# Kernel optimization log

Hardware: AMD Instinct MI355X
Metric: run time of the kernel (lower is better)

Reference implementation:

```python
import jax, jax.numpy as jnp
import numpy as np

N_PATCHES = 14  # per side -> 196 patches

def patchify(images, n_patches):
    # images: [n, c, h, w]; returns [n, n_patches**2, c*ps*ps] with flatten order (c, ph, pw)
    n, c, h, w = images.shape
    ps = h // n_patches
    x = images.reshape(n, c, n_patches, ps, n_patches, ps)
    x = x.transpose(0, 2, 4, 1, 3, 5)  # [n, np_i, np_j, c, ps, ps]
    return x.reshape(n, n_patches * n_patches, c * ps * ps)

def setup_inputs() -> dict:
    key = jax.random.key(0)
    k1, k2, k3, k4 = jax.random.split(key, 4)
    B, C, H, Wd = 64, 3, 224, 224
    input_d = C * (H // N_PATCHES) * (Wd // N_PATCHES)  # 768
    hidden_d = 768
    images = jax.random.normal(k1, (B, C, H, Wd), dtype=jnp.float32)
    W = jax.random.normal(k2, (hidden_d, input_d), dtype=jnp.float32) * (1.0 / np.sqrt(input_d))
    b = jax.random.normal(k3, (hidden_d,), dtype=jnp.float32) * 0.01
    class_token = jax.random.uniform(k4, (1, hidden_d), dtype=jnp.float32)
    return {"images": images, "W": W, "b": b, "class_token": class_token}

def reference(images, W, b, class_token):
    patches = patchify(images, N_PATCHES)               # [B, 196, 768]
    tokens = jnp.einsum('bpd,hd->bph', patches, W) + b  # linear_mapper
    B = tokens.shape[0]
    cls = jnp.broadcast_to(class_token[None, :, :], (B, 1, class_token.shape[-1]))
    return jnp.concatenate([cls, tokens], axis=1)       # [B, 197, hidden_d]
```

## Files before the change

### kernel.cpp

```cpp
#include <hip/hip_runtime.h>
#include <cstdint>
#include <cstddef>

#define MTOT 12544
#define KTOT 768
#define NTOT 768

typedef float  f32x4  __attribute__((ext_vector_type(4)));
typedef __bf16 bf16x8 __attribute__((ext_vector_type(8)));

#define IMG_ELEMS (64*3*224*224)
#define W_ELEMS   (768*768)
#define A_BLOCKS  (IMG_ELEMS/8/256)
#define W_BLOCKS  (W_ELEMS/8/256)
#define CLS_BLOCKS 48

__global__ __launch_bounds__(256) void prep_kernel(
    const float* __restrict__ images, const float* __restrict__ Wm,
    const float* __restrict__ cls, float* __restrict__ out,
    __bf16* __restrict__ imgb, __bf16* __restrict__ Wb) {
  const int bid = blockIdx.x, tid = threadIdx.x;
  if (bid < A_BLOCKS) {
    const size_t q = (size_t)bid * 256 + tid;
    const float4 v0 = *(const float4*)(images + q * 8);
    const float4 v1 = *(const float4*)(images + q * 8 + 4);
    bf16x8 o;
    o[0]=(__bf16)v0.x; o[1]=(__bf16)v0.y; o[2]=(__bf16)v0.z; o[3]=(__bf16)v0.w;
    o[4]=(__bf16)v1.x; o[5]=(__bf16)v1.y; o[6]=(__bf16)v1.z; o[7]=(__bf16)v1.w;
    *(bf16x8*)(imgb + q * 8) = o;
  } else if (bid < A_BLOCKS + W_BLOCKS) {
    const size_t q = (size_t)(bid - A_BLOCKS) * 256 + tid;
    const float4 v0 = *(const float4*)(Wm + q * 8);
    const float4 v1 = *(const float4*)(Wm + q * 8 + 4);
    bf16x8 o;
    o[0]=(__bf16)v0.x; o[1]=(__bf16)v0.y; o[2]=(__bf16)v0.z; o[3]=(__bf16)v0.w;
    o[4]=(__bf16)v1.x; o[5]=(__bf16)v1.y; o[6]=(__bf16)v1.z; o[7]=(__bf16)v1.w;
    *(bf16x8*)(Wb + q * 8) = o;
  } else {
    const int t  = (bid - A_BLOCKS - W_BLOCKS) * 256 + tid;
    const int bb = t / 192;
    const int r  = t - bb * 192;
    *(float4*)(out + (size_t)bb * 197 * 768 + r * 4) = *(const float4*)(cls + r * 4);
  }
}

#define BM 64
#define BN 128
#define BK 64
#define NBLK_N 6
#define NWG   1176
#define WG_PER_XCD 147

__device__ __forceinline__ void gload_lds16(const void* g, void* l) {
  __builtin_amdgcn_global_load_lds((__attribute__((address_space(1))) void*)(g),
                                   (__attribute__((address_space(3))) void*)(l),
                                   16, 0, 0);
}

__global__ __launch_bounds__(256) void gemm_kernel(
    const __bf16* __restrict__ imgb, const __bf16* __restrict__ Wb,
    const float* __restrict__ bias, float* __restrict__ out) {
  __shared__ __bf16 As[2 * 64 * 32];
  __shared__ __bf16 Bs[2 * 128 * 32];

  const int tid  = threadIdx.x;
  const int bx   = blockIdx.x;
  const int wgid = (bx & 7) * WG_PER_XCD + (bx >> 3);
  const int mblk = wgid / NBLK_N;
  const int nblk = wgid - mblk * NBLK_N;
  const int m0 = mblk * BM;
  const int n0 = nblk * BN;
  const int wave = tid >> 6, lane = tid & 63;
  const int wm = (wave & 1) * 32;
  const int wn = (wave >> 1) * 64;
  const int lrow = lane & 15, lq = lane >> 4;

  f32x4 acc[2][4] = {};

  const __bf16* pA[2];
#pragma unroll
  for (int s = 0; s < 2; ++s) {
    const int c = wave * 128 + s * 64 + lane;
    const int kstep = c >> 8, rem = c & 255;
    const int row = rem >> 2, jc = rem & 3;
    const int m = m0 + row;
    const int bb = m / 196, p = m - bb * 196;
    const int pi = p / 14, pj = p - pi * 14;
    const int ph_off = kstep * 2 + (jc >> 1);
    const int pw_off = (jc & 1) * 8;
    const size_t e = ((size_t)(bb * 3 * 224 + pi * 16 + ph_off)) * 224 + pj * 16 + pw_off;
    pA[s] = imgb + e;
  }
  const __bf16* pB[4];
#pragma unroll
  for (int s = 0; s < 4; ++s) {
    const int c = wave * 256 + s * 64 + lane;
    const int kstep = c >> 9, rem = c & 511;
    const int h = rem >> 2, jc = rem & 3;
    pB[s] = Wb + (size_t)(n0 + h) * 768 + kstep * 32 + jc * 8;
  }
  __bf16* lA[2];
  __bf16* lB[4];
#pragma unroll
  for (int s = 0; s < 2; ++s) lA[s] = As + (wave * 128 + s * 64) * 8;
#pragma unroll
  for (int s = 0; s < 4; ++s) lB[s] = Bs + (wave * 256 + s * 64) * 8;

  for (int kt = 0; kt < KTOT / BK; ++kt) {
#pragma unroll
    for (int s = 0; s < 2; ++s) gload_lds16(pA[s], lA[s]);
#pragma unroll
    for (int s = 0; s < 4; ++s) gload_lds16(pB[s], lB[s]);
    const int dA = ((kt & 3) == 3) ? 47488 : 896;
    pA[0] += dA; pA[1] += dA;
    pB[0] += BK; pB[1] += BK; pB[2] += BK; pB[3] += BK;
    __syncthreads();

#pragma unroll
    for (int ks = 0; ks < 2; ++ks) {
      bf16x8 af[2], bf[4];
#pragma unroll
      for (int i = 0; i < 2; ++i)
        af[i] = *(const bf16x8*)&As[ks * 2048 + (wm + i * 16 + lrow) * 32 + lq * 8];
#pragma unroll
      for (int j = 0; j < 4; ++j)
        bf[j] = *(const bf16x8*)&Bs[ks * 4096 + (wn + j * 16 + lrow) * 32 + lq * 8];
#pragma unroll
      for (int i = 0; i < 2; ++i)
#pragma unroll
        for (int j = 0; j < 4; ++j)
          acc[i][j] = __builtin_amdgcn_mfma_f32_16x16x32_bf16(af[i], bf[j], acc[i][j], 0, 0, 0);
    }
    __syncthreads();
  }

#pragma unroll
  for (int j = 0; j < 4; ++j) {
    const int h  = n0 + wn + j * 16 + lrow;
    const float bv = bias[h];
#pragma unroll
    for (int i = 0; i < 2; ++i) {
      const int mb = m0 + wm + i * 16 + lq * 4;
#pragma unroll
      for (int r = 0; r < 4; ++r) {
        const int m  = mb + r;
        const int bb = m / 196, p = m - bb * 196;
        out[(size_t)(bb * 197 + 1 + p) * 768 + h] = acc[i][j][r] + bv;
      }
    }
  }
}

extern "C" void kernel_launch(void* const* d_in, const int* in_sizes, int n_in,
                              void* d_out, int out_size, void* d_ws, size_t ws_size,
                              hipStream_t stream) {
  const float* images = (const float*)d_in[0];
  const float* Wm     = (const float*)d_in[1];
  const float* b      = (const float*)d_in[2];
  const float* cls    = (const float*)d_in[3];
  float* out = (float*)d_out;

  __bf16* imgb = (__bf16*)d_ws;
  __bf16* Wb   = imgb + (size_t)IMG_ELEMS;
  (void)in_sizes; (void)n_in; (void)out_size; (void)ws_size;

  prep_kernel<<<A_BLOCKS + W_BLOCKS + CLS_BLOCKS, 256, 0, stream>>>(
      images, Wm, cls, out, imgb, Wb);
  gemm_kernel<<<NWG, 256, 0, stream>>>(imgb, Wb, b, out);
}
```

Baseline: 112.8 us.

## Double-buffer LDS tiles to prefetch next K-tile during MFMA compute

Doubles the A and B shared-memory buffers and restructures the K loop into a prologue, a steady-state loop and an epilogue. Each iteration issues the global_load_lds for the next tile into the alternate buffer before running the MFMAs on the current one, so load latency can overlap compute. It also removes one barrier per iteration. The cost is twice the LDS per workgroup, which may reduce how many workgroups fit on a CU.

```diff
diff --git a/kernel.cpp b/kernel.cpp
--- a/kernel.cpp
+++ b/kernel.cpp
@@ -60,8 +60,8 @@
 __global__ __launch_bounds__(256) void gemm_kernel(
     const __bf16* __restrict__ imgb, const __bf16* __restrict__ Wb,
     const float* __restrict__ bias, float* __restrict__ out) {
-  __shared__ __bf16 As[2 * 64 * 32];
-  __shared__ __bf16 Bs[2 * 128 * 32];
+  __shared__ __bf16 As[2 * 64 * 32 * 2];
+  __shared__ __bf16 Bs[2 * 128 * 32 * 2];
 
   const int tid  = threadIdx.x;
   const int bx   = blockIdx.x;
@@ -99,40 +99,61 @@
     const int h = rem >> 2, jc = rem & 3;
     pB[s] = Wb + (size_t)(n0 + h) * 768 + kstep * 32 + jc * 8;
   }
-  __bf16* lA[2];
-  __bf16* lB[4];
+  __bf16* lA[2][2];
+  __bf16* lB[2][4];
 #pragma unroll
-  for (int s = 0; s < 2; ++s) lA[s] = As + (wave * 128 + s * 64) * 8;
+  for (int s = 0; s < 2; ++s) {
+    const int off = (wave * 128 + s * 64) * 8;
+    lA[0][s] = As + off; lA[1][s] = As + 4096 + off;
+  }
 #pragma unroll
-  for (int s = 0; s < 4; ++s) lB[s] = Bs + (wave * 256 + s * 64) * 8;
+  for (int s = 0; s < 4; ++s) {
+    const int off = (wave * 256 + s * 64) * 8;
+    lB[0][s] = Bs + off; lB[1][s] = Bs + 8192 + off;
+  }
 
-  for (int kt = 0; kt < KTOT / BK; ++kt) {
-#pragma unroll
-    for (int s = 0; s < 2; ++s) gload_lds16(pA[s], lA[s]);
-#pragma unroll
-    for (int s = 0; s < 4; ++s) gload_lds16(pB[s], lB[s]);
-    const int dA = ((kt & 3) == 3) ? 47488 : 896;
-    pA[0] += dA; pA[1] += dA;
-    pB[0] += BK; pB[1] += BK; pB[2] += BK; pB[3] += BK;
-    __syncthreads();
-
+  auto compute = [&](int cur) {
+    const __bf16* Ab = As + cur * 4096;
+    const __bf16* Bb = Bs + cur * 8192;
 #pragma unroll
     for (int ks = 0; ks < 2; ++ks) {
       bf16x8 af[2], bf[4];
 #pragma unroll
       for (int i = 0; i < 2; ++i)
-        af[i] = *(const bf16x8*)&As[ks * 2048 + (wm + i * 16 + lrow) * 32 + lq * 8];
+        af[i] = *(const bf16x8*)&Ab[ks * 2048 + (wm + i * 16 + lrow) * 32 + lq * 8];
 #pragma unroll
       for (int j = 0; j < 4; ++j)
-        bf[j] = *(const bf16x8*)&Bs[ks * 4096 + (wn + j * 16 + lrow) * 32 + lq * 8];
+        bf[j] = *(const bf16x8*)&Bb[ks * 4096 + (wn + j * 16 + lrow) * 32 + lq * 8];
 #pragma unroll
       for (int i = 0; i < 2; ++i)
 #pragma unroll
         for (int j = 0; j < 4; ++j)
           acc[i][j] = __builtin_amdgcn_mfma_f32_16x16x32_bf16(af[i], bf[j], acc[i][j], 0, 0, 0);
     }
+  };
+
+#pragma unroll
+  for (int s = 0; s < 2; ++s) gload_lds16(pA[s], lA[0][s]);
+#pragma unroll
+  for (int s = 0; s < 4; ++s) gload_lds16(pB[s], lB[0][s]);
+  pA[0] += 896; pA[1] += 896;
+  pB[0] += BK; pB[1] += BK; pB[2] += BK; pB[3] += BK;
+  __syncthreads();
+
+  for (int kt = 0; kt < KTOT / BK - 1; ++kt) {
+    const int cur = kt & 1, nxt = cur ^ 1;
+#pragma unroll
+    for (int s = 0; s < 2; ++s) gload_lds16(pA[s], lA[nxt][s]);
+#pragma unroll
+    for (int s = 0; s < 4; ++s) gload_lds16(pB[s], lB[nxt][s]);
+    const int dA = (((kt + 1) & 3) == 3) ? 47488 : 896;
+    pA[0] += dA; pA[1] += dA;
+    pB[0] += BK; pB[1] += BK; pB[2] += BK; pB[3] += BK;
+
+    compute(cur);
     __syncthreads();
   }
+  compute(1);
 
 #pragma unroll
   for (int j = 0; j < 4; ++j) {
```

Result: slower. 118.2 us (+4.7%).

## Double-buffer GEMM k-loop with BK=32 to overlap LDS loads and MFMA

Applied to the files above, without the earlier changes.

Halves the k-tile to 32 and double-buffers A/B shared tiles, issuing the async global-to-LDS load for the next tile before computing on the current one. This aims to hide global load latency behind MFMA work and cut barriers per k element. It doubles the number of k iterations and relies on barrier-implied waits for the async LDS loads to complete.

```diff
diff --git a/kernel.cpp b/kernel.cpp
--- a/kernel.cpp
+++ b/kernel.cpp
@@ -46,7 +46,8 @@
 
 #define BM 64
 #define BN 128
-#define BK 64
+#define BK 32
+#define NKT 24
 #define NBLK_N 6
 #define NWG   1176
 #define WG_PER_XCD 147
@@ -60,8 +61,8 @@
 __global__ __launch_bounds__(256) void gemm_kernel(
     const __bf16* __restrict__ imgb, const __bf16* __restrict__ Wb,
     const float* __restrict__ bias, float* __restrict__ out) {
-  __shared__ __bf16 As[2 * 64 * 32];
-  __shared__ __bf16 Bs[2 * 128 * 32];
+  __shared__ __bf16 As[2][BM * BK];
+  __shared__ __bf16 Bs[2][BN * BK];
 
   const int tid  = threadIdx.x;
   const int bx   = blockIdx.x;
@@ -77,62 +78,64 @@
 
   f32x4 acc[2][4] = {};
 
-  const __bf16* pA[2];
+  const __bf16* pA;
+  {
+    const int row = tid >> 2, jc = tid & 3;
+    const int m = m0 + row;
+    const int bb = m / 196, p = m - bb * 196;
+    const int pi = p / 14, pj = p - pi * 14;
+    pA = imgb + ((size_t)(bb * 3 * 224 + pi * 16 + (jc >> 1))) * 224 + pj * 16 + (jc & 1) * 8;
+  }
+  const __bf16* pB[2];
+  int cB[2];
 #pragma unroll
   for (int s = 0; s < 2; ++s) {
     const int c = wave * 128 + s * 64 + lane;
-    const int kstep = c >> 8, rem = c & 255;
-    const int row = rem >> 2, jc = rem & 3;
-    const int m = m0 + row;
-    const int bb = m / 196, p = m - bb * 196;
-    const int pi = p / 14, pj = p - pi * 14;
-    const int ph_off = kstep * 2 + (jc >> 1);
-    const int pw_off = (jc & 1) * 8;
-    const size_t e = ((size_t)(bb * 3 * 224 + pi * 16 + ph_off)) * 224 + pj * 16 + pw_off;
-    pA[s] = imgb + e;
+    cB[s] = c;
+    const int h = c >> 2, jc = c & 3;
+    pB[s] = Wb + (size_t)(n0 + h) * 768 + jc * 8;
   }
-  const __bf16* pB[4];
+
+  auto stage = [&](int b) {
+    gload_lds16(pA, (void*)(As[b] + tid * 8));
+    gload_lds16(pB[0], (void*)(Bs[b] + cB[0] * 8));
+    gload_lds16(pB[1], (void*)(Bs[b] + cB[1] * 8));
+  };
+  auto advance = [&](int t) {
+    const int dA = ((t & 7) == 7) ? 47040 : 448;
+    pA += dA; pB[0] += BK; pB[1] += BK;
+  };
+  auto compute = [&](int b) {
+    bf16x8 af[2], bf[4];
 #pragma unroll
-  for (int s = 0; s < 4; ++s) {
-    const int c = wave * 256 + s * 64 + lane;
-    const int kstep = c >> 9, rem = c & 511;
-    const int h = rem >> 2, jc = rem & 3;
-    pB[s] = Wb + (size_t)(n0 + h) * 768 + kstep * 32 + jc * 8;
-  }
-  __bf16* lA[2];
-  __bf16* lB[4];
+    for (int i = 0; i < 2; ++i)
+      af[i] = *(const bf16x8*)&As[b][(wm + i * 16 + lrow) * 32 + lq * 8];
 #pragma unroll
-  for (int s = 0; s < 2; ++s) lA[s] = As + (wave * 128 + s * 64) * 8;
+    for (int j = 0; j < 4; ++j)
+      bf[j] = *(const bf16x8*)&Bs[b][(wn + j * 16 + lrow) * 32 + lq * 8];
 #pragma unroll
-  for (int s = 0; s < 4; ++s) lB[s] = Bs + (wave * 256 + s * 64) * 8;
-
-  for (int kt = 0; kt < KTOT / BK; ++kt) {
-#pragma unroll
-    for (int s = 0; s < 2; ++s) gload_lds16(pA[s], lA[s]);
-#pragma unroll
-    for (int s = 0; s < 4; ++s) gload_lds16(pB[s], lB[s]);
-    const int dA = ((kt & 3) == 3) ? 47488 : 896;
-    pA[0] += dA; pA[1] += dA;
-    pB[0] += BK; pB[1] += BK; pB[2] += BK; pB[3] += BK;
-    __syncthreads();
-
-#pragma unroll
-    for (int ks = 0; ks < 2; ++ks) {
-      bf16x8 af[2], bf[4];
-#pragma unroll
-      for (int i = 0; i < 2; ++i)
-        af[i] = *(const bf16x8*)&As[ks * 2048 + (wm + i * 16 + lrow) * 32 + lq * 8];
+    for (int i = 0; i < 2; ++i)
 #pragma unroll
       for (int j = 0; j < 4; ++j)
-        bf[j] = *(const bf16x8*)&Bs[ks * 4096 + (wn + j * 16 + lrow) * 32 + lq * 8];
-#pragma unroll
-      for (int i = 0; i < 2; ++i)
-#pragma unroll
-        for (int j = 0; j < 4; ++j)
-          acc[i][j] = __builtin_amdgcn_mfma_f32_16x16x32_bf16(af[i], bf[j], acc[i][j], 0, 0, 0);
-    }
+        acc[i][j] = __builtin_amdgcn_mfma_f32_16x16x32_bf16(af[i], bf[j], acc[i][j], 0, 0, 0);
+  };
+
+  stage(0); advance(0);
+  __syncthreads();
+
+  for (int i = 0; i < 11; ++i) {
+    const int t = 2 * i + 1;
+    stage(1); advance(t);
+    compute(0);
+    __syncthreads();
+    stage(0); advance(t + 1);
+    compute(1);
     __syncthreads();
   }
+  stage(1);
+  compute(0);
+  __syncthreads();
+  compute(1);
 
 #pragma unroll
   for (int j = 0; j < 4; ++j) {
```

New measurement: 117.4 us. +4.1%, slower.
